# Kernel tuning notes

Hardware: AMD Instinct MI355X
Metric: run time of the kernel (lower is better)

The kernel has to match this reference:

```python
import jax, jax.numpy as jnp
import numpy as np

HOP = 512
FAC = 4
FRAME_LEN = FAC * HOP  # 2048
ALPHA = 0.65
BETA = 0.06


def _inverse_stft_window():
    # torch.hann_window (periodic): w[n] = 0.5*(1 - cos(2*pi*n/N))
    n = np.arange(FRAME_LEN)
    w = 0.5 * (1.0 - np.cos(2.0 * np.pi * n / FRAME_LEN))
    denom = w ** 2
    # overlaps = ceil(frame_length / hop) == FAC (frame_length = FAC*HOP exactly)
    denom = denom.reshape(FAC, HOP).sum(axis=0)          # [HOP]
    denom = np.tile(denom, FAC)                          # [FRAME_LEN]
    return (w / denom).astype(np.float32)


def setup_inputs() -> dict:
    key = jax.random.key(0)
    B, F, T = 8, 1024, 2048
    stft_frames = jax.random.normal(key, (B, 2, F, T), dtype=jnp.float32)
    inv_window = jnp.asarray(_inverse_stft_window())
    return {"stft_frames": stft_frames, "inv_window": inv_window}


def reference(stft_frames, inv_window):
    # stft_frames: [B, 2, F, T] (real/imag stacked on dim 1)
    x = jnp.pad(stft_frames, ((0, 0), (0, 0), (0, 1), (0, 0)))  # F -> F+1 (Nyquist bin)
    real = x[:, 0] / BETA   # [B, F+1, T]
    imag = x[:, 1] / BETA
    # denormalize_complex: |x|^(1/alpha) * exp(i * atan2(im, re))
    mag = (real * real + imag * imag) ** (0.5 / ALPHA)
    theta = jnp.arctan2(imag, real)
    spec = jax.lax.complex(mag * jnp.cos(theta), mag * jnp.sin(theta))  # [B, F+1, T]
    frames = jnp.fft.irfft(spec, axis=-2)                 # [B, 2F, T], 2F == FRAME_LEN
    frames = jnp.transpose(frames, (0, 2, 1))             # [B, T, L]
    frames = frames * inv_window[None, None, :]
    B, T, L = frames.shape
    total = (T - 1) * HOP + L
    # vectorized overlap-add (scatter-add replacing the per-frame python loop)
    idx = (jnp.arange(T)[:, None] * HOP + jnp.arange(L)[None, :]).reshape(-1)  # [T*L]
    full = jnp.zeros((B, total), frames.dtype).at[:, idx].add(frames.reshape(B, -1))
    # output_buffer is empty on the first call; chunk = first hop*T samples
    return full[:, : HOP * T]
```

## Files before the change

kernel.cpp:

```cpp
#include <hip/hip_runtime.h>
#include <cstddef>


#define TDIM 2048
#define FDIM 1024
#define TT 8
#define NTOT (512 * 2048)

static constexpr int kBREV[32] = {0,16,8,24,4,20,12,28,2,18,10,26,6,22,14,30,
                                  1,17,9,25,5,21,13,29,3,19,11,27,7,23,15,31};
static constexpr float kTR[16] = {
  1.0f, 0.98078528040323044f, 0.92387953251128674f, 0.83146961230254524f,
  0.70710678118654757f, 0.55557023301960218f, 0.38268343236508978f, 0.19509032201612825f,
  0.0f, -0.19509032201612825f, -0.38268343236508978f, -0.55557023301960218f,
  -0.70710678118654757f, -0.83146961230254524f, -0.92387953251128674f, -0.98078528040323044f};
static constexpr float kTI[16] = {
  0.0f, 0.19509032201612825f, 0.38268343236508978f, 0.55557023301960218f,
  0.70710678118654757f, 0.83146961230254524f, 0.92387953251128674f, 0.98078528040323044f,
  1.0f, 0.98078528040323044f, 0.92387953251128674f, 0.83146961230254524f,
  0.70710678118654757f, 0.55557023301960218f, 0.38268343236508978f, 0.19509032201612825f};
static constexpr float kCC[32] = {
  1.0f, 0.99518472667219693f, 0.98078528040323044f, 0.95694033573220882f,
  0.92387953251128674f, 0.88192126434835505f, 0.83146961230254524f, 0.77301045336273699f,
  0.70710678118654757f, 0.63439328416364549f, 0.55557023301960218f, 0.47139673682599764f,
  0.38268343236508978f, 0.29028467725446233f, 0.19509032201612825f, 0.098017140329560604f,
  0.0f, -0.098017140329560604f, -0.19509032201612825f, -0.29028467725446233f,
  -0.38268343236508978f, -0.47139673682599764f, -0.55557023301960218f, -0.63439328416364549f,
  -0.70710678118654757f, -0.77301045336273699f, -0.83146961230254524f, -0.88192126434835505f,
  -0.92387953251128674f, -0.95694033573220882f, -0.98078528040323044f, -0.99518472667219693f};
static constexpr float kSS[32] = {
  0.0f, 0.098017140329560604f, 0.19509032201612825f, 0.29028467725446233f,
  0.38268343236508978f, 0.47139673682599764f, 0.55557023301960218f, 0.63439328416364549f,
  0.70710678118654757f, 0.77301045336273699f, 0.83146961230254524f, 0.88192126434835505f,
  0.92387953251128674f, 0.95694033573220882f, 0.98078528040323044f, 0.99518472667219693f,
  1.0f, 0.99518472667219693f, 0.98078528040323044f, 0.95694033573220882f,
  0.92387953251128674f, 0.88192126434835505f, 0.83146961230254524f, 0.77301045336273699f,
  0.70710678118654757f, 0.63439328416364549f, 0.55557023301960218f, 0.47139673682599764f,
  0.38268343236508978f, 0.29028467725446233f, 0.19509032201612825f, 0.098017140329560604f};

template <int H>
__device__ __forceinline__ void fft32_stage(float ar[32], float ai[32]) {
  constexpr int TSTEP = 16 / H;
  #pragma unroll
  for (int g = 0; g < 32; g += 2 * H) {
    #pragma unroll
    for (int j = 0; j < H; ++j) {
      const float twr = kTR[j * TSTEP];
      const float twi = kTI[j * TSTEP];
      const int i0 = g + j, i1 = i0 + H;
      const float tr = twr * ar[i1] - twi * ai[i1];
      const float ti = twr * ai[i1] + twi * ar[i1];
      ar[i1] = ar[i0] - tr; ai[i1] = ai[i0] - ti;
      ar[i0] += tr;         ai[i0] += ti;
    }
  }
}

__device__ __forceinline__ void ifft32_core(float ar[32], float ai[32]) {
  fft32_stage<1>(ar, ai);
  fft32_stage<2>(ar, ai);
  fft32_stage<4>(ar, ai);
  fft32_stage<8>(ar, ai);
  fft32_stage<16>(ar, ai);
}

__device__ __forceinline__ float pow_gain(float v, float PE, float KS) {
  return KS * __builtin_amdgcn_exp2f(PE * __builtin_amdgcn_logf(v));
}

#define XH(t, k1, rh) ((k1) * 132 + (rh) * 8 + (t))
#define FSTR 2053

__global__ __launch_bounds__(256) void istft_fused(const float* __restrict__ in,
                                                   const float* __restrict__ invw,
                                                   float* __restrict__ out) {
  __shared__ float buf[8448];
  float* Xhr = buf;
  float* Xhi = buf + 4224;
  float* Fh  = buf;

  const int tid = threadIdx.x;
  const int tl  = tid & 7;
  const int q   = tid >> 3;

  const int id   = blockIdx.x;
  const int xcd  = id & 7;
  const int slot = id >> 3;
  const int b    = slot >> 5;
  const int tile = xcd * 32 + (slot & 31);
  const int t0   = tile * TT;
  const int t    = t0 + tl;

  const float* re_p = in + ((size_t)b * 2 + 0) * ((size_t)FDIM * TDIM);
  const float* im_p = in + ((size_t)b * 2 + 1) * ((size_t)FDIM * TDIM);

  const float KS = (float)(exp((-1.0 / 0.65) * log(0.06)) / 2048.0);
  const float PE = 7.0f / 26.0f;

  float ar[32], ai[32];
  {
    const float aq = 3.0679615757712824e-3f * (float)q;
    const float wc = __cosf(aq), ws = __sinf(aq);
    #pragma unroll
    for (int k2 = 0; k2 < 32; ++k2) {
      const int k  = q + 32 * k2;
      const int km = (1024 - k) & 1023;
      const float x1 = re_p[(size_t)k  * TDIM + t];
      const float y1 = im_p[(size_t)k  * TDIM + t];
      const float x2 = re_p[(size_t)km * TDIM + t];
      const float y2 = im_p[(size_t)km * TDIM + t];
      const float g1 = pow_gain(x1 * x1 + y1 * y1, PE, KS);
      const float g2 = pow_gain(x2 * x2 + y2 * y2, PE, KS);
      const float s1r = x1 * g1, s1i = y1 * g1;
      const float s2r = x2 * g2, s2i = y2 * g2;
      const float cs = wc * kCC[k2] - ws * kSS[k2];
      const float sn = ws * kCC[k2] + wc * kSS[k2];
      const float Pre = s1r + s2r, Pim = s1i - s2i;
      const float Qre = s1r - s2r, Qim = s1i + s2i;
      const float u = cs * Qim + sn * Qre;
      const float v = cs * Qre - sn * Qim;
      float wr = Pre - u, wi = Pim + v;
      if (q == 0 && k2 == 0) { wr = s1r; wi = s1r; }
      ar[kBREV[k2]] = wr; ai[kBREV[k2]] = wi;
    }
    ifft32_core(ar, ai);
  }

  float zr[32], zi[32];
  #pragma unroll
  for (int r = 0; r < 16; ++r) {
    const float ang = 6.1359231515425649e-3f * (float)(q * r);
    const float sn = __sinf(ang), cs = __cosf(ang);
    Xhr[XH(tl, q, r)] = cs * ar[r] - sn * ai[r];
    Xhi[XH(tl, q, r)] = cs * ai[r] + sn * ar[r];
  }
  __syncthreads();
  if (q < 16) {
    #pragma unroll
    for (int i = 0; i < 32; ++i) {
      zr[i] = Xhr[XH(tl, kBREV[i], q)];
      zi[i] = Xhi[XH(tl, kBREV[i], q)];
    }
  }
  __syncthreads();
  #pragma unroll
  for (int r = 16; r < 32; ++r) {
    const float ang = 6.1359231515425649e-3f * (float)(q * r);
    const float sn = __sinf(ang), cs = __cosf(ang);
    Xhr[XH(tl, q, r - 16)] = cs * ar[r] - sn * ai[r];
    Xhi[XH(tl, q, r - 16)] = cs * ai[r] + sn * ar[r];
  }
  __syncthreads();
  if (q >= 16) {
    #pragma unroll
    for (int i = 0; i < 32; ++i) {
      zr[i] = Xhr[XH(tl, kBREV[i], q - 16)];
      zi[i] = Xhi[XH(tl, kBREV[i], q - 16)];
    }
  }
  __syncthreads();

  ifft32_core(zr, zi);

  float* ob = out + (size_t)b * NTOT;
  float acc[3][2];

  if (tl < 4) {
    #pragma unroll
    for (int s = 0; s < 32; ++s) {
      const int l0 = 2 * q + 64 * s;
      Fh[tl * FSTR + l0]     = zr[s] * invw[l0];
      Fh[tl * FSTR + l0 + 1] = zi[s] * invw[l0 + 1];
    }
  }
  __syncthreads();
  #pragma unroll
  for (int rel = 0; rel < 7; ++rel) {
    #pragma unroll
    for (int half = 0; half < 2; ++half) {
      const int j = tid + 256 * half;
      float v = 0.0f;
      #pragma unroll
      for (int c = 0; c < 4; ++c) {
        const int tt = rel - c;
        if (tt >= 0 && tt < 4) v += Fh[tt * FSTR + j + 512 * c];
      }
      if (rel < 3)       atomicAdd(&ob[(t0 + rel) * 512 + j], v);
      else if (rel == 3) ob[(t0 + rel) * 512 + j] = v;
      else               acc[rel - 4][half] = v;
    }
  }
  __syncthreads();
  if (tl >= 4) {
    #pragma unroll
    for (int s = 0; s < 32; ++s) {
      const int l0 = 2 * q + 64 * s;
      Fh[(tl - 4) * FSTR + l0]     = zr[s] * invw[l0];
      Fh[(tl - 4) * FSTR + l0 + 1] = zi[s] * invw[l0 + 1];
    }
  }
  __syncthreads();
  #pragma unroll
  for (int rel = 4; rel < 11; ++rel) {
    const int tp = t0 + rel;
    if (tp > 2047) continue;
    #pragma unroll
    for (int half = 0; half < 2; ++half) {
      const int j = tid + 256 * half;
      float v = (rel < 7) ? acc[rel - 4][half] : 0.0f;
      #pragma unroll
      for (int c = 0; c < 4; ++c) {
        const int tt = rel - c;
        if (tt >= 4 && tt < 8) v += Fh[(tt - 4) * FSTR + j + 512 * c];
      }
      const int n = tp * 512 + j;
      if (rel <= 7) ob[n] = v;
      else atomicAdd(&ob[n], v);
    }
  }
}

extern "C" void kernel_launch(void* const* d_in, const int* in_sizes, int n_in,
                              void* d_out, int out_size, void* d_ws, size_t ws_size,
                              hipStream_t stream) {
  (void)in_sizes; (void)n_in; (void)d_ws; (void)ws_size;
  const float* in   = (const float*)d_in[0];
  const float* invw = (const float*)d_in[1];
  float* out = (float*)d_out;
  hipMemsetAsync(out, 0, (size_t)out_size * sizeof(float), stream);
  istft_fused<<<dim3(TDIM / TT * 8), 256, 0, stream>>>(in, invw, out);
}
```

Measured before the change: 246.2 us.

## Stage input loads through shared memory with float4 coalesced reads and single denorm

Input spectra are now loaded cooperatively with float4 vector loads across 8 time columns and staged into shared memory in two halves. Each bin is denormalized once instead of twice, since the mirrored bin pair was previously loaded and processed separately per thread. The first FFT stage then reads both bins from LDS. The goal is to cut redundant global loads and transcendental math and improve coalescing, at the cost of extra barriers and LDS traffic.

```diff
diff --git a/kernel.cpp b/kernel.cpp
--- a/kernel.cpp
+++ b/kernel.cpp
@@ -6,6 +6,7 @@
 #define FDIM 1024
 #define TT 8
 #define NTOT (512 * 2048)
+#define SPLANE 4224
 
 static constexpr int kBREV[32] = {0,16,8,24,4,20,12,28,2,18,10,26,6,22,14,30,
                                   1,17,9,25,5,21,13,29,3,19,11,27,7,23,15,31};
@@ -68,6 +69,48 @@
   return KS * __builtin_amdgcn_exp2f(PE * __builtin_amdgcn_logf(v));
 }
 
+__device__ __forceinline__ void denorm4(float4& r, float4& i, float PE, float KS) {
+  float g;
+  g = pow_gain(r.x * r.x + i.x * i.x, PE, KS); r.x *= g; i.x *= g;
+  g = pow_gain(r.y * r.y + i.y * i.y, PE, KS); r.y *= g; i.y *= g;
+  g = pow_gain(r.z * r.z + i.z * i.z, PE, KS); r.z *= g; i.z *= g;
+  g = pow_gain(r.w * r.w + i.w * i.w, PE, KS); r.w *= g; i.w *= g;
+}
+
+template <int SC>
+__device__ __forceinline__ int slot_row(int s) {
+  return (SC == 0) ? (s < 256 ? s : s + 512) : (s + 256);
+}
+
+template <int SC>
+__device__ __forceinline__ void stage1_compute(const float* __restrict__ Sre,
+                                               const float* __restrict__ Sim,
+                                               int q, int tl, float wc, float ws,
+                                               float ar[32], float ai[32]) {
+  #pragma unroll
+  for (int u = 0; u < 16; ++u) {
+    const int k2 = (SC == 0) ? (u < 8 ? u : u + 16) : (u + 8);
+    const int slot = q + 32 * u;
+    int slotm_zero = 32 * (16 - u);
+    if (SC == 0 && u == 0) slotm_zero = 0;
+    if (SC == 0 && u == 8) slotm_zero = 512;
+    const int slotm_pos = (32 - q) + 32 * (15 - u);
+    const int slotm = (q == 0) ? slotm_zero : slotm_pos;
+
+    const float s1r = Sre[slot * 8 + tl],  s1i = Sim[slot * 8 + tl];
+    const float s2r = Sre[slotm * 8 + tl], s2i = Sim[slotm * 8 + tl];
+    const float cs = wc * kCC[k2] - ws * kSS[k2];
+    const float sn = ws * kCC[k2] + wc * kSS[k2];
+    const float Pre = s1r + s2r, Pim = s1i - s2i;
+    const float Qre = s1r - s2r, Qim = s1i + s2i;
+    const float uu = cs * Qim + sn * Qre;
+    const float vv = cs * Qre - sn * Qim;
+    float wr = Pre - uu, wi = Pim + vv;
+    if (q == 0 && k2 == 0) { wr = s1r; wi = s1r; }
+    ar[kBREV[k2]] = wr; ai[kBREV[k2]] = wi;
+  }
+}
+
 #define XH(t, k1, rh) ((k1) * 132 + (rh) * 8 + (t))
 #define FSTR 2053
 
@@ -75,6 +118,8 @@
                                                    const float* __restrict__ invw,
                                                    float* __restrict__ out) {
   __shared__ float buf[8448];
+  float* Sre = buf;
+  float* Sim = buf + SPLANE;
   float* Xhr = buf;
   float* Xhi = buf + 4224;
   float* Fh  = buf;
@@ -89,7 +134,6 @@
   const int b    = slot >> 5;
   const int tile = xcd * 32 + (slot & 31);
   const int t0   = tile * TT;
-  const int t    = t0 + tl;
 
   const float* re_p = in + ((size_t)b * 2 + 0) * ((size_t)FDIM * TDIM);
   const float* im_p = in + ((size_t)b * 2 + 1) * ((size_t)FDIM * TDIM);
@@ -97,34 +141,76 @@
   const float KS = (float)(exp((-1.0 / 0.65) * log(0.06)) / 2048.0);
   const float PE = 7.0f / 26.0f;
 
+  const float aq = 3.0679615757712824e-3f * (float)q;
+  const float wc = __cosf(aq), ws = __sinf(aq);
+
   float ar[32], ai[32];
-  {
-    const float aq = 3.0679615757712824e-3f * (float)q;
-    const float wc = __cosf(aq), ws = __sinf(aq);
-    #pragma unroll
-    for (int k2 = 0; k2 < 32; ++k2) {
-      const int k  = q + 32 * k2;
-      const int km = (1024 - k) & 1023;
-      const float x1 = re_p[(size_t)k  * TDIM + t];
-      const float y1 = im_p[(size_t)k  * TDIM + t];
-      const float x2 = re_p[(size_t)km * TDIM + t];
-      const float y2 = im_p[(size_t)km * TDIM + t];
-      const float g1 = pow_gain(x1 * x1 + y1 * y1, PE, KS);
-      const float g2 = pow_gain(x2 * x2 + y2 * y2, PE, KS);
-      const float s1r = x1 * g1, s1i = y1 * g1;
-      const float s2r = x2 * g2, s2i = y2 * g2;
-      const float cs = wc * kCC[k2] - ws * kSS[k2];
-      const float sn = ws * kCC[k2] + wc * kSS[k2];
-      const float Pre = s1r + s2r, Pim = s1i - s2i;
-      const float Qre = s1r - s2r, Qim = s1i + s2i;
-      const float u = cs * Qim + sn * Qre;
-      const float v = cs * Qre - sn * Qim;
-      float wr = Pre - u, wi = Pim + v;
-      if (q == 0 && k2 == 0) { wr = s1r; wi = s1r; }
-      ar[kBREV[k2]] = wr; ai[kBREV[k2]] = wi;
-    }
-    ifft32_core(ar, ai);
-  }
+
+  float4 reA[4], imA[4];
+  #pragma unroll
+  for (int j = 0; j < 4; ++j) {
+    const int f = tid + 256 * j;
+    const int s = f >> 1, cg = f & 1;
+    const int row = slot_row<0>(s);
+    reA[j] = *(const float4*)(re_p + (size_t)row * TDIM + t0 + 4 * cg);
+    imA[j] = *(const float4*)(im_p + (size_t)row * TDIM + t0 + 4 * cg);
+  }
+  float4 exRe, exIm;
+  if (tid < 2) {
+    exRe = *(const float4*)(re_p + (size_t)256 * TDIM + t0 + 4 * tid);
+    exIm = *(const float4*)(im_p + (size_t)256 * TDIM + t0 + 4 * tid);
+  }
+  #pragma unroll
+  for (int j = 0; j < 4; ++j) {
+    const int f = tid + 256 * j;
+    const int s = f >> 1, cg = f & 1;
+    denorm4(reA[j], imA[j], PE, KS);
+    *(float4*)(Sre + s * 8 + 4 * cg) = reA[j];
+    *(float4*)(Sim + s * 8 + 4 * cg) = imA[j];
+  }
+  if (tid < 2) {
+    denorm4(exRe, exIm, PE, KS);
+    *(float4*)(Sre + 512 * 8 + 4 * tid) = exRe;
+    *(float4*)(Sim + 512 * 8 + 4 * tid) = exIm;
+  }
+
+  float4 reB[4], imB[4];
+  #pragma unroll
+  for (int j = 0; j < 4; ++j) {
+    const int f = tid + 256 * j;
+    const int s = f >> 1, cg = f & 1;
+    const int row = slot_row<1>(s);
+    reB[j] = *(const float4*)(re_p + (size_t)row * TDIM + t0 + 4 * cg);
+    imB[j] = *(const float4*)(im_p + (size_t)row * TDIM + t0 + 4 * cg);
+  }
+  float4 exReB, exImB;
+  if (tid < 2) {
+    exReB = *(const float4*)(re_p + (size_t)768 * TDIM + t0 + 4 * tid);
+    exImB = *(const float4*)(im_p + (size_t)768 * TDIM + t0 + 4 * tid);
+  }
+  __syncthreads();
+
+  stage1_compute<0>(Sre, Sim, q, tl, wc, ws, ar, ai);
+  __syncthreads();
+
+  #pragma unroll
+  for (int j = 0; j < 4; ++j) {
+    const int f = tid + 256 * j;
+    const int s = f >> 1, cg = f & 1;
+    denorm4(reB[j], imB[j], PE, KS);
+    *(float4*)(Sre + s * 8 + 4 * cg) = reB[j];
+    *(float4*)(Sim + s * 8 + 4 * cg) = imB[j];
+  }
+  if (tid < 2) {
+    denorm4(exReB, exImB, PE, KS);
+    *(float4*)(Sre + 512 * 8 + 4 * tid) = exReB;
+    *(float4*)(Sim + 512 * 8 + 4 * tid) = exImB;
+  }
+  __syncthreads();
+  stage1_compute<1>(Sre, Sim, q, tl, wc, ws, ar, ai);
+  __syncthreads();
+
+  ifft32_core(ar, ai);
 
   float zr[32], zi[32];
   #pragma unroll
```

New measurement: 227.8 us. 1.08x faster.

## Stage spectrum loads through LDS with float4 coalescing and shrink shared memory

Applied to the files above, without the earlier changes.

The input load is restructured. Threads now cooperatively load float4-vectorized, coalesced chunks of spectrum rows into shared memory, with the next chunk loaded while the current one is computed. Denormalization happens once per element instead of twice, since the mirrored bin is read from LDS rather than reloaded and recomputed. The transpose and overlap-add phases are split into four passes over a smaller LDS buffer, which cuts shared memory to about 17 KB to raise occupancy, at the cost of more __syncthreads barriers.

```diff
diff --git a/kernel.cpp b/kernel.cpp
--- a/kernel.cpp
+++ b/kernel.cpp
@@ -6,6 +6,9 @@
 #define FDIM 1024
 #define TT 8
 #define NTOT (512 * 2048)
+#define SPL 2064
+#define XPL 2176
+#define FST 2054
 
 static constexpr int kBREV[32] = {0,16,8,24,4,20,12,28,2,18,10,26,6,22,14,30,
                                   1,17,9,25,5,21,13,29,3,19,11,27,7,23,15,31};
@@ -68,15 +71,104 @@
   return KS * __builtin_amdgcn_exp2f(PE * __builtin_amdgcn_logf(v));
 }
 
-#define XH(t, k1, rh) ((k1) * 132 + (rh) * 8 + (t))
-#define FSTR 2053
+__device__ __forceinline__ void denorm4(float4& r, float4& i, float PE, float KS) {
+  float g;
+  g = pow_gain(r.x * r.x + i.x * i.x, PE, KS); r.x *= g; i.x *= g;
+  g = pow_gain(r.y * r.y + i.y * i.y, PE, KS); r.y *= g; i.y *= g;
+  g = pow_gain(r.z * r.z + i.z * i.z, PE, KS); r.z *= g; i.z *= g;
+  g = pow_gain(r.w * r.w + i.w * i.w, PE, KS); r.w *= g; i.w *= g;
+}
+
+template <int C>
+__device__ __forceinline__ int chunk_k2(int u) {
+  return (C == 3) ? 12 + u : (u < 4 ? 4 * C + u : 24 - 4 * C + u);
+}
+
+template <int C>
+__device__ __forceinline__ void chunk_load(const float* __restrict__ re_p,
+                                           const float* __restrict__ im_p,
+                                           int t0, int tid,
+                                           float4 re[2], float4 im[2],
+                                           float4& exr, float4& exi) {
+  #pragma unroll
+  for (int j = 0; j < 2; ++j) {
+    const int f = tid + 256 * j;
+    const int s = f >> 1, cg = f & 1;
+    const int row = 32 * chunk_k2<C>(s >> 5) + (s & 31);
+    re[j] = *(const float4*)(re_p + (size_t)row * TDIM + t0 + 4 * cg);
+    im[j] = *(const float4*)(im_p + (size_t)row * TDIM + t0 + 4 * cg);
+  }
+  constexpr int NE = (C == 1 || C == 2) ? 2 : 1;
+  if (tid < 2 * NE) {
+    const int er = tid >> 1, cg = tid & 1;
+    const int row = (C == 0) ? 128
+                  : (C == 1) ? (er ? 896 : 256)
+                  : (C == 2) ? (er ? 768 : 384) : 640;
+    exr = *(const float4*)(re_p + (size_t)row * TDIM + t0 + 4 * cg);
+    exi = *(const float4*)(im_p + (size_t)row * TDIM + t0 + 4 * cg);
+  }
+}
+
+template <int C>
+__device__ __forceinline__ void chunk_stage(float* __restrict__ Sre,
+                                            float* __restrict__ Sim, int tid,
+                                            float4 re[2], float4 im[2],
+                                            float4& exr, float4& exi,
+                                            float PE, float KS) {
+  #pragma unroll
+  for (int j = 0; j < 2; ++j) {
+    const int f = tid + 256 * j;
+    denorm4(re[j], im[j], PE, KS);
+    *(float4*)(Sre + 4 * f) = re[j];
+    *(float4*)(Sim + 4 * f) = im[j];
+  }
+  constexpr int NE = (C == 1 || C == 2) ? 2 : 1;
+  if (tid < 2 * NE) {
+    denorm4(exr, exi, PE, KS);
+    *(float4*)(Sre + 2048 + 4 * tid) = exr;
+    *(float4*)(Sim + 2048 + 4 * tid) = exi;
+  }
+}
+
+template <int C>
+__device__ __forceinline__ void chunk_compute(const float* __restrict__ Sre,
+                                              const float* __restrict__ Sim,
+                                              int q, int tl, float wc, float ws,
+                                              float ar[32], float ai[32]) {
+  constexpr int E0 = (C == 0) ? 0 : (C == 3) ? 256 : 257;
+  constexpr int E4 = (C == 3) ? 128 : 256;
+  #pragma unroll
+  for (int u = 0; u < 8; ++u) {
+    const int k2 = chunk_k2<C>(u);
+    const int slot = q + 32 * u;
+    const int slotm_z = (u == 0) ? E0 : (u == 4) ? E4 : 32 * (8 - u);
+    const int slotm_p = (32 - q) + 32 * (7 - u);
+    const int slotm = (q == 0) ? slotm_z : slotm_p;
+
+    const float s1r = Sre[slot * 8 + tl],  s1i = Sim[slot * 8 + tl];
+    const float s2r = Sre[slotm * 8 + tl], s2i = Sim[slotm * 8 + tl];
+    const float cs = wc * kCC[k2] - ws * kSS[k2];
+    const float sn = ws * kCC[k2] + wc * kSS[k2];
+    const float Pre = s1r + s2r, Pim = s1i - s2i;
+    const float Qre = s1r - s2r, Qim = s1i + s2i;
+    const float uu = cs * Qim + sn * Qre;
+    const float vv = cs * Qre - sn * Qim;
+    float wr = Pre - uu, wi = Pim + vv;
+    if (C == 0 && u == 0 && q == 0) { wr = s1r; wi = s1r; }
+    ar[kBREV[k2]] = wr; ai[kBREV[k2]] = wi;
+  }
+}
+
+#define XQ(t, k1, rh) ((k1) * 68 + (rh) * 8 + (t))
 
 __global__ __launch_bounds__(256) void istft_fused(const float* __restrict__ in,
                                                    const float* __restrict__ invw,
                                                    float* __restrict__ out) {
-  __shared__ float buf[8448];
-  float* Xhr = buf;
-  float* Xhi = buf + 4224;
+  __shared__ float buf[4352];
+  float* Sre = buf;
+  float* Sim = buf + SPL;
+  float* Xqr = buf;
+  float* Xqi = buf + XPL;
   float* Fh  = buf;
 
   const int tid = threadIdx.x;
@@ -89,7 +181,6 @@
   const int b    = slot >> 5;
   const int tile = xcd * 32 + (slot & 31);
   const int t0   = tile * TT;
-  const int t    = t0 + tl;
 
   const float* re_p = in + ((size_t)b * 2 + 0) * ((size_t)FDIM * TDIM);
   const float* im_p = in + ((size_t)b * 2 + 1) * ((size_t)FDIM * TDIM);
@@ -97,126 +188,104 @@
   const float KS = (float)(exp((-1.0 / 0.65) * log(0.06)) / 2048.0);
   const float PE = 7.0f / 26.0f;
 
+  const float aq = 3.0679615757712824e-3f * (float)q;
+  const float wc = __cosf(aq), ws = __sinf(aq);
+
   float ar[32], ai[32];
+
   {
-    const float aq = 3.0679615757712824e-3f * (float)q;
-    const float wc = __cosf(aq), ws = __sinf(aq);
+    float4 reA[2], imA[2], exrA, exiA;
+    float4 reB[2], imB[2], exrB, exiB;
+    chunk_load<0>(re_p, im_p, t0, tid, reA, imA, exrA, exiA);
+    chunk_stage<0>(Sre, Sim, tid, reA, imA, exrA, exiA, PE, KS);
+    chunk_load<1>(re_p, im_p, t0, tid, reB, imB, exrB, exiB);
+    __syncthreads();
+    chunk_compute<0>(Sre, Sim, q, tl, wc, ws, ar, ai);
+    __syncthreads();
+    chunk_stage<1>(Sre, Sim, tid, reB, imB, exrB, exiB, PE, KS);
+    chunk_load<2>(re_p, im_p, t0, tid, reA, imA, exrA, exiA);
+    __syncthreads();
+    chunk_compute<1>(Sre, Sim, q, tl, wc, ws, ar, ai);
+    __syncthreads();
+    chunk_stage<2>(Sre, Sim, tid, reA, imA, exrA, exiA, PE, KS);
+    chunk_load<3>(re_p, im_p, t0, tid, reB, imB, exrB, exiB);
+    __syncthreads();
+    chunk_compute<2>(Sre, Sim, q, tl, wc, ws, ar, ai);
+    __syncthreads();
+    chunk_stage<3>(Sre, Sim, tid, reB, imB, exrB, exiB, PE, KS);
+    __syncthreads();
+    chunk_compute<3>(Sre, Sim, q, tl, wc, ws, ar, ai);
+    __syncthreads();
+  }
+
+  ifft32_core(ar, ai);
+
+  float zr[32], zi[32];
+  #pragma unroll
+  for (int p = 0; p < 4; ++p) {
     #pragma unroll
-    for (int k2 = 0; k2 < 32; ++k2) {
-      const int k  = q + 32 * k2;
-      const int km = (1024 - k) & 1023;
-      const float x1 = re_p[(size_t)k  * TDIM + t];
-      const float y1 = im_p[(size_t)k  * TDIM + t];
-      const float x2 = re_p[(size_t)km * TDIM + t];
-      const float y2 = im_p[(size_t)km * TDIM + t];
-      const float g1 = pow_gain(x1 * x1 + y1 * y1, PE, KS);
-      const float g2 = pow_gain(x2 * x2 + y2 * y2, PE, KS);
-      const float s1r = x1 * g1, s1i = y1 * g1;
-      const float s2r = x2 * g2, s2i = y2 * g2;
-      const float cs = wc * kCC[k2] - ws * kSS[k2];
-      const float sn = ws * kCC[k2] + wc * kSS[k2];
-      const float Pre = s1r + s2r, Pim = s1i - s2i;
-      const float Qre = s1r - s2r, Qim = s1i + s2i;
-      const float u = cs * Qim + sn * Qre;
-      const float v = cs * Qre - sn * Qim;
-      float wr = Pre - u, wi = Pim + v;
-      if (q == 0 && k2 == 0) { wr = s1r; wi = s1r; }
-      ar[kBREV[k2]] = wr; ai[kBREV[k2]] = wi;
-    }
-    ifft32_core(ar, ai);
-  }
-
-  float zr[32], zi[32];
-  #pragma unroll
-  for (int r = 0; r < 16; ++r) {
-    const float ang = 6.1359231515425649e-3f * (float)(q * r);
-    const float sn = __sinf(ang), cs = __cosf(ang);
-    Xhr[XH(tl, q, r)] = cs * ar[r] - sn * ai[r];
-    Xhi[XH(tl, q, r)] = cs * ai[r] + sn * ar[r];
-  }
-  __syncthreads();
-  if (q < 16) {
-    #pragma unroll
-    for (int i = 0; i < 32; ++i) {
-      zr[i] = Xhr[XH(tl, kBREV[i], q)];
-      zi[i] = Xhi[XH(tl, kBREV[i], q)];
-    }
-  }
-  __syncthreads();
-  #pragma unroll
-  for (int r = 16; r < 32; ++r) {
-    const float ang = 6.1359231515425649e-3f * (float)(q * r);
-    const float sn = __sinf(ang), cs = __cosf(ang);
-    Xhr[XH(tl, q, r - 16)] = cs * ar[r] - sn * ai[r];
-    Xhi[XH(tl, q, r - 16)] = cs * ai[r] + sn * ar[r];
-  }
-  __syncthreads();
-  if (q >= 16) {
-    #pragma unroll
-    for (int i = 0; i < 32; ++i) {
-      zr[i] = Xhr[XH(tl, kBREV[i], q - 16)];
-      zi[i] = Xhi[XH(tl, kBREV[i], q - 16)];
-    }
-  }
-  __syncthreads();
+    for (int rr = 0; rr < 8; ++rr) {
+      const int r = 8 * p + rr;
+      const float ang = 6.1359231515425649e-3f * (float)(q * r);
+      const float sn = __sinf(ang), cs = __cosf(ang);
+      Xqr[XQ(tl, q, rr)] = cs * ar[r] - sn * ai[r];
+      Xqi[XQ(tl, q, rr)] = cs * ai[r] + sn * ar[r];
+    }
+    __syncthreads();
+    if ((q >> 3) == p) {
+      const int qq = q & 7;
+      #pragma unroll
+      for (int i = 0; i < 32; ++i) {
+        zr[i] = Xqr[XQ(tl, kBREV[i], qq)];
+        zi[i] = Xqi[XQ(tl, kBREV[i], qq)];
+      }
+    }
+    __syncthreads();
+  }
 
   ifft32_core(zr, zi);
 
   float* ob = out + (size_t)b * NTOT;
-  float acc[3][2];
-
-  if (tl < 4) {
-    #pragma unroll
-    for (int s = 0; s < 32; ++s) {
-      const int l0 = 2 * q + 64 * s;
-      Fh[tl * FSTR + l0]     = zr[s] * invw[l0];
-      Fh[tl * FSTR + l0 + 1] = zi[s] * invw[l0 + 1];
-    }
-  }
-  __syncthreads();
-  #pragma unroll
-  for (int rel = 0; rel < 7; ++rel) {
+  float carry[2][3];
+
+  #pragma unroll
+  for (int p = 0; p < 4; ++p) {
+    if ((tl >> 1) == p) {
+      const int row = tl & 1;
+      #pragma unroll
+      for (int s = 0; s < 32; ++s) {
+        const int l0 = 2 * q + 64 * s;
+        const float2 w2 = *(const float2*)(invw + l0);
+        float2 fv; fv.x = zr[s] * w2.x; fv.y = zi[s] * w2.y;
+        *(float2*)(Fh + row * FST + l0) = fv;
+      }
+    }
+    __syncthreads();
     #pragma unroll
     for (int half = 0; half < 2; ++half) {
       const int j = tid + 256 * half;
-      float v = 0.0f;
       #pragma unroll
-      for (int c = 0; c < 4; ++c) {
-        const int tt = rel - c;
-        if (tt >= 0 && tt < 4) v += Fh[tt * FSTR + j + 512 * c];
+      for (int rel = 2 * p; rel < 2 * p + 5 && rel < 11; ++rel) {
+        float v = (p > 0 && rel - 2 * p < 3) ? carry[half][rel - 2 * p] : 0.0f;
+        #pragma unroll
+        for (int c = 0; c < 4; ++c) {
+          const int tt = rel - c;
+          if (tt == 2 * p || tt == 2 * p + 1)
+            v += Fh[(tt - 2 * p) * FST + j + 512 * c];
+        }
+        if (rel <= 2 * p + 1 || p == 3) {
+          const int tp = t0 + rel;
+          if (rel < 8 || tp <= 2047) {
+            const int n = tp * 512 + j;
+            if (rel >= 3 && rel <= 7) ob[n] = v;
+            else atomicAdd(&ob[n], v);
+          }
+        } else {
+          carry[half][rel - (2 * p + 2)] = v;
+        }
       }
-      if (rel < 3)       atomicAdd(&ob[(t0 + rel) * 512 + j], v);
-      else if (rel == 3) ob[(t0 + rel) * 512 + j] = v;
-      else               acc[rel - 4][half] = v;
-    }
-  }
-  __syncthreads();
-  if (tl >= 4) {
-    #pragma unroll
-    for (int s = 0; s < 32; ++s) {
-      const int l0 = 2 * q + 64 * s;
-      Fh[(tl - 4) * FSTR + l0]     = zr[s] * invw[l0];
-      Fh[(tl - 4) * FSTR + l0 + 1] = zi[s] * invw[l0 + 1];
-    }
-  }
-  __syncthreads();
-  #pragma unroll
-  for (int rel = 4; rel < 11; ++rel) {
-    const int tp = t0 + rel;
-    if (tp > 2047) continue;
-    #pragma unroll
-    for (int half = 0; half < 2; ++half) {
-      const int j = tid + 256 * half;
-      float v = (rel < 7) ? acc[rel - 4][half] : 0.0f;
-      #pragma unroll
-      for (int c = 0; c < 4; ++c) {
-        const int tt = rel - c;
-        if (tt >= 4 && tt < 8) v += Fh[(tt - 4) * FSTR + j + 512 * c];
-      }
-      const int n = tp * 512 + j;
-      if (rel <= 7) ob[n] = v;
-      else atomicAdd(&ob[n], v);
-    }
+    }
+    if (p < 3) __syncthreads();
   }
 }
 
```

New measurement: 260.5 us. 5.8% more time.

## Stage input spectrum through LDS with vectorized loads and double-buffered chunks

Applied to the files above, without the earlier changes.

Replaces per-thread scalar strided global loads (each bin read twice, once as k and once as its mirror) with cooperative float4 loads of row chunks into shared memory. The denormalization gain is computed once per bin instead of twice. Chunks are double-buffered so the next chunk's global loads overlap the current chunk's pairing math. This adds extra barriers and LDS traffic and raises register pressure from the prefetched float4 buffers.

```diff
diff --git a/kernel.cpp b/kernel.cpp
--- a/kernel.cpp
+++ b/kernel.cpp
@@ -6,6 +6,7 @@
 #define FDIM 1024
 #define TT 8
 #define NTOT (512 * 2048)
+#define SPL 2064
 
 static constexpr int kBREV[32] = {0,16,8,24,4,20,12,28,2,18,10,26,6,22,14,30,
                                   1,17,9,25,5,21,13,29,3,19,11,27,7,23,15,31};
@@ -68,6 +69,94 @@
   return KS * __builtin_amdgcn_exp2f(PE * __builtin_amdgcn_logf(v));
 }
 
+__device__ __forceinline__ void denorm4(float4& r, float4& i, float PE, float KS) {
+  float g;
+  g = pow_gain(r.x * r.x + i.x * i.x, PE, KS); r.x *= g; i.x *= g;
+  g = pow_gain(r.y * r.y + i.y * i.y, PE, KS); r.y *= g; i.y *= g;
+  g = pow_gain(r.z * r.z + i.z * i.z, PE, KS); r.z *= g; i.z *= g;
+  g = pow_gain(r.w * r.w + i.w * i.w, PE, KS); r.w *= g; i.w *= g;
+}
+
+template <int C>
+__device__ __forceinline__ int chunk_k2(int u) {
+  return (C == 3) ? 12 + u : (u < 4 ? 4 * C + u : 24 - 4 * C + u);
+}
+
+template <int C>
+__device__ __forceinline__ void chunk_load(const float* __restrict__ re_p,
+                                           const float* __restrict__ im_p,
+                                           int t0, int tid,
+                                           float4 re[2], float4 im[2],
+                                           float4& exr, float4& exi) {
+  #pragma unroll
+  for (int j = 0; j < 2; ++j) {
+    const int f = tid + 256 * j;
+    const int s = f >> 1, cg = f & 1;
+    const int row = 32 * chunk_k2<C>(s >> 5) + (s & 31);
+    re[j] = *(const float4*)(re_p + (size_t)row * TDIM + t0 + 4 * cg);
+    im[j] = *(const float4*)(im_p + (size_t)row * TDIM + t0 + 4 * cg);
+  }
+  constexpr int NE = (C == 1 || C == 2) ? 2 : 1;
+  if (tid < 2 * NE) {
+    const int er = tid >> 1, cg = tid & 1;
+    const int row = (C == 0) ? 128
+                  : (C == 1) ? (er ? 896 : 256)
+                  : (C == 2) ? (er ? 768 : 384) : 640;
+    exr = *(const float4*)(re_p + (size_t)row * TDIM + t0 + 4 * cg);
+    exi = *(const float4*)(im_p + (size_t)row * TDIM + t0 + 4 * cg);
+  }
+}
+
+template <int C>
+__device__ __forceinline__ void chunk_stage(float* __restrict__ Sre,
+                                            float* __restrict__ Sim, int tid,
+                                            float4 re[2], float4 im[2],
+                                            float4& exr, float4& exi,
+                                            float PE, float KS) {
+  #pragma unroll
+  for (int j = 0; j < 2; ++j) {
+    const int f = tid + 256 * j;
+    denorm4(re[j], im[j], PE, KS);
+    *(float4*)(Sre + 4 * f) = re[j];
+    *(float4*)(Sim + 4 * f) = im[j];
+  }
+  constexpr int NE = (C == 1 || C == 2) ? 2 : 1;
+  if (tid < 2 * NE) {
+    denorm4(exr, exi, PE, KS);
+    *(float4*)(Sre + 2048 + 4 * tid) = exr;
+    *(float4*)(Sim + 2048 + 4 * tid) = exi;
+  }
+}
+
+template <int C>
+__device__ __forceinline__ void chunk_compute(const float* __restrict__ Sre,
+                                              const float* __restrict__ Sim,
+                                              int q, int tl, float wc, float ws,
+                                              float ar[32], float ai[32]) {
+  constexpr int E0 = (C == 0) ? 0 : (C == 3) ? 256 : 257;
+  constexpr int E4 = (C == 3) ? 128 : 256;
+  #pragma unroll
+  for (int u = 0; u < 8; ++u) {
+    const int k2 = chunk_k2<C>(u);
+    const int slot = q + 32 * u;
+    const int slotm_z = (u == 0) ? E0 : (u == 4) ? E4 : 32 * (8 - u);
+    const int slotm_p = (32 - q) + 32 * (7 - u);
+    const int slotm = (q == 0) ? slotm_z : slotm_p;
+
+    const float s1r = Sre[slot * 8 + tl],  s1i = Sim[slot * 8 + tl];
+    const float s2r = Sre[slotm * 8 + tl], s2i = Sim[slotm * 8 + tl];
+    const float cs = wc * kCC[k2] - ws * kSS[k2];
+    const float sn = ws * kCC[k2] + wc * kSS[k2];
+    const float Pre = s1r + s2r, Pim = s1i - s2i;
+    const float Qre = s1r - s2r, Qim = s1i + s2i;
+    const float uu = cs * Qim + sn * Qre;
+    const float vv = cs * Qre - sn * Qim;
+    float wr = Pre - uu, wi = Pim + vv;
+    if (C == 0 && u == 0 && q == 0) { wr = s1r; wi = s1r; }
+    ar[kBREV[k2]] = wr; ai[kBREV[k2]] = wi;
+  }
+}
+
 #define XH(t, k1, rh) ((k1) * 132 + (rh) * 8 + (t))
 #define FSTR 2053
 
@@ -89,7 +178,6 @@
   const int b    = slot >> 5;
   const int tile = xcd * 32 + (slot & 31);
   const int t0   = tile * TT;
-  const int t    = t0 + tl;
 
   const float* re_p = in + ((size_t)b * 2 + 0) * ((size_t)FDIM * TDIM);
   const float* im_p = in + ((size_t)b * 2 + 1) * ((size_t)FDIM * TDIM);
@@ -97,34 +185,37 @@
   const float KS = (float)(exp((-1.0 / 0.65) * log(0.06)) / 2048.0);
   const float PE = 7.0f / 26.0f;
 
+  const float aq = 3.0679615757712824e-3f * (float)q;
+  const float wc = __cosf(aq), ws = __sinf(aq);
+
   float ar[32], ai[32];
+
   {
-    const float aq = 3.0679615757712824e-3f * (float)q;
-    const float wc = __cosf(aq), ws = __sinf(aq);
-    #pragma unroll
-    for (int k2 = 0; k2 < 32; ++k2) {
-      const int k  = q + 32 * k2;
-      const int km = (1024 - k) & 1023;
-      const float x1 = re_p[(size_t)k  * TDIM + t];
-      const float y1 = im_p[(size_t)k  * TDIM + t];
-      const float x2 = re_p[(size_t)km * TDIM + t];
-      const float y2 = im_p[(size_t)km * TDIM + t];
-      const float g1 = pow_gain(x1 * x1 + y1 * y1, PE, KS);
-      const float g2 = pow_gain(x2 * x2 + y2 * y2, PE, KS);
-      const float s1r = x1 * g1, s1i = y1 * g1;
-      const float s2r = x2 * g2, s2i = y2 * g2;
-      const float cs = wc * kCC[k2] - ws * kSS[k2];
-      const float sn = ws * kCC[k2] + wc * kSS[k2];
-      const float Pre = s1r + s2r, Pim = s1i - s2i;
-      const float Qre = s1r - s2r, Qim = s1i + s2i;
-      const float u = cs * Qim + sn * Qre;
-      const float v = cs * Qre - sn * Qim;
-      float wr = Pre - u, wi = Pim + v;
-      if (q == 0 && k2 == 0) { wr = s1r; wi = s1r; }
-      ar[kBREV[k2]] = wr; ai[kBREV[k2]] = wi;
-    }
-    ifft32_core(ar, ai);
-  }
+    float* S0r = buf;         float* S0i = buf + SPL;
+    float* S1r = buf + 4224;  float* S1i = buf + 4224 + SPL;
+    float4 rA[2], iA[2], exrA, exiA;
+    float4 rB[2], iB[2], exrB, exiB;
+
+    chunk_load<0>(re_p, im_p, t0, tid, rA, iA, exrA, exiA);
+    chunk_stage<0>(S0r, S0i, tid, rA, iA, exrA, exiA, PE, KS);
+    chunk_load<1>(re_p, im_p, t0, tid, rB, iB, exrB, exiB);
+    __syncthreads();
+    chunk_load<2>(re_p, im_p, t0, tid, rA, iA, exrA, exiA);
+    chunk_stage<1>(S1r, S1i, tid, rB, iB, exrB, exiB, PE, KS);
+    chunk_compute<0>(S0r, S0i, q, tl, wc, ws, ar, ai);
+    __syncthreads();
+    chunk_load<3>(re_p, im_p, t0, tid, rB, iB, exrB, exiB);
+    chunk_stage<2>(S0r, S0i, tid, rA, iA, exrA, exiA, PE, KS);
+    chunk_compute<1>(S1r, S1i, q, tl, wc, ws, ar, ai);
+    __syncthreads();
+    chunk_stage<3>(S1r, S1i, tid, rB, iB, exrB, exiB, PE, KS);
+    chunk_compute<2>(S0r, S0i, q, tl, wc, ws, ar, ai);
+    __syncthreads();
+    chunk_compute<3>(S1r, S1i, q, tl, wc, ws, ar, ai);
+    __syncthreads();
+  }
+
+  ifft32_core(ar, ai);
 
   float zr[32], zi[32];
   #pragma unroll
```

Result: faster. 228.4 us (-7.2%).
